# Kernel optimization log

Hardware: AMD Instinct MI355X
Metric: run time of the kernel (lower is better)

## Reference

```python
import jax, jax.numpy as jnp
import numpy as np

N = 300000   # total nodes
C = 32       # hidden states
M = 64       # discrete label alphabet
NGEN = 8     # number of generative models
G = 8192     # number of graphs


def setup_inputs() -> dict:
    key = jax.random.key(0)
    k1, k2, k3, k4 = jax.random.split(key, 4)
    B = jax.random.uniform(k1, (C, M, NGEN), minval=-5.0, maxval=5.0, dtype=jnp.float32)
    Pi = jax.random.uniform(k2, (C, NGEN), minval=-5.0, maxval=5.0, dtype=jnp.float32)
    x = jax.random.randint(k3, (N,), 0, M)
    batch = jnp.sort(jax.random.randint(k4, (N,), 0, G))
    return {"B": B, "Pi": Pi, "x": x, "batch": batch, "num_graphs": G}


def reference(B, Pi, x, batch, num_graphs):
    # softmax reparameterization: over M for B, over C for Pi (per generator)
    sm_B = jax.nn.softmax(B, axis=1)          # (C, M, n_gen)
    sm_Pi = jax.nn.softmax(Pi, axis=0)        # (C, n_gen)
    # gather per-node emission probs, then joint with prior -> (N, C, n_gen)
    numerator = sm_Pi[None, :, :] * jnp.transpose(sm_B[:, x, :], (1, 0, 2))
    posterior = numerator / numerator.sum(axis=1, keepdims=True)  # (N, C, n_gen)
    likelihood = (posterior * jnp.log(numerator)).sum(axis=1)     # (N, n_gen)
    # scatter-sum per graph
    likelihood = jax.ops.segment_sum(likelihood, batch, num_segments=num_graphs)  # (G, n_gen)
    h_vals = posterior.max(axis=1, keepdims=True)   # (N, 1, n_gen)
    h_idx = posterior.argmax(axis=1)                # (N, n_gen)
    return likelihood, h_vals, h_idx
```

## Files before the change

kernel.cpp:

```cpp
#include <hip/hip_runtime.h>

#define C_DIM 32
#define M_DIM 64
#define NG    8
#define TAB   (M_DIM * NG)
#define ST    9
#define BST   520
#define SPB   2048

__global__ void __launch_bounds__(512)
cgmm_prep(const float* __restrict__ B, const float* __restrict__ Pi,
          const int* __restrict__ batch,
          float* __restrict__ tab, int* __restrict__ starts,
          int N, int G, int nsb) {
    const int tid = threadIdx.x;

    if ((int)blockIdx.x < nsb) {
        const int base = blockIdx.x * SPB;
        for (int i = tid; i < SPB; i += 512) {
            const int n = base + i;
            if (n >= N) break;
            const int bn = batch[n];
            if (n == 0) {
                for (int j = 0; j <= bn; ++j) starts[j] = 0;
            } else {
                const int bp = batch[n - 1];
                for (int j = bp + 1; j <= bn; ++j) starts[j] = n;
            }
            if (n == N - 1) {
                for (int j = bn + 1; j <= G; ++j) starts[j] = N;
            }
        }
        return;
    }

    __shared__ float Bs[C_DIM * BST];
    __shared__ float Pis[C_DIM * NG];
    __shared__ float lsePi_s[NG];
    __shared__ float K_s[C_DIM * NG];

    {
        const float4* B4 = (const float4*)B;
        float4* Bs4 = (float4*)Bs;
        #pragma unroll
        for (int i = tid; i < (C_DIM * M_DIM * NG) / 4; i += 512) {
            Bs4[(i >> 7) * (BST / 4) + (i & 127)] = B4[i];
        }
        if (tid < C_DIM * NG / 4) ((float4*)Pis)[tid] = ((const float4*)Pi)[tid];
    }
    __syncthreads();

    if (tid < NG) {
        float mx = -1e30f;
        #pragma unroll
        for (int c = 0; c < C_DIM; ++c) mx = fmaxf(mx, Pis[c * NG + tid]);
        float s = 0.f;
        #pragma unroll
        for (int c = 0; c < C_DIM; ++c) s += expf(Pis[c * NG + tid] - mx);
        lsePi_s[tid] = logf(s) + mx;
    }
    __syncthreads();

    if (tid < C_DIM * NG) {
        const int c = tid >> 3, g = tid & 7;
        const float* bp = Bs + c * BST + g;
        float mx = -1e30f;
        #pragma unroll
        for (int m = 0; m < M_DIM; ++m) mx = fmaxf(mx, bp[m * NG]);
        float s = 0.f;
        #pragma unroll
        for (int m = 0; m < M_DIM; ++m) s += expf(bp[m * NG] - mx);
        K_s[tid] = Pis[tid] - (logf(s) + mx) - lsePi_s[g];
    }
    __syncthreads();

    {
        const int m = tid >> 3, g = tid & 7;
        float L[C_DIM];
        float best = -1e30f; int bidx = 0;
        #pragma unroll
        for (int c = 0; c < C_DIM; ++c) {
            float v = Bs[c * BST + m * NG + g] + K_s[c * NG + g];
            L[c] = v;
            if (v > best) { best = v; bidx = c; }
        }
        float se = 0.f, la = 0.f;
        #pragma unroll
        for (int c = 0; c < C_DIM; ++c) {
            float e = expf(L[c] - best);
            se += e; la += e * L[c];
        }
        tab[tid]           = la / se;
        tab[TAB + tid]     = 1.f / se;
        tab[2 * TAB + tid] = (float)bidx;
    }
}

__global__ void __launch_bounds__(256)
cgmm_write(const int* __restrict__ x, const int* __restrict__ starts,
           const float* __restrict__ tab,
           float* __restrict__ out_like, float* __restrict__ out_hv,
           float* __restrict__ out_hi, int G) {
    __shared__ float like_s[M_DIM * ST];
    __shared__ float hval_s[M_DIM * ST];
    __shared__ float hidx_s[M_DIM * ST];
    const int tid = threadIdx.x;
    for (int i = tid; i < TAB; i += 256) {
        const int p = (i >> 3) * ST + (i & 7);
        like_s[p] = tab[i];
        hval_s[p] = tab[TAB + i];
        hidx_s[p] = tab[2 * TAB + i];
    }
    __syncthreads();

    const int j = blockIdx.x * 4 + (tid >> 6);
    if (j >= G) return;
    const int start = starts[j];
    const int end   = starts[j + 1];

    const int slot = (tid >> 3) & 7;
    const int g    = tid & 7;

    float acc = 0.f;
    for (int n = start + slot; n < end; n += 8) {
        const int xm = x[n];
        const int p  = xm * ST + g;
        acc += like_s[p];
        out_hv[(size_t)n * NG + g] = hval_s[p];
        out_hi[(size_t)n * NG + g] = hidx_s[p];
    }
    acc += __shfl_xor(acc, 8);
    acc += __shfl_xor(acc, 16);
    acc += __shfl_xor(acc, 32);
    if ((tid & 63) < NG) out_like[(size_t)j * NG + g] = acc;
}

extern "C" void kernel_launch(void* const* d_in, const int* in_sizes, int n_in,
                              void* d_out, int out_size, void* d_ws, size_t ws_size,
                              hipStream_t stream) {
    const float* B     = (const float*)d_in[0];
    const float* Pi    = (const float*)d_in[1];
    const int*   x     = (const int*)d_in[2];
    const int*   batch = (const int*)d_in[3];
    const int N = in_sizes[2];
    const int G = (out_size - 2 * N * NG) / NG;

    float* tab    = (float*)d_ws;
    int*   starts = (int*)((char*)d_ws + 8192);

    float* out_like = (float*)d_out;
    float* out_hv   = out_like + (size_t)G * NG;
    float* out_hi   = out_hv + (size_t)N * NG;

    const int nsb = (N + SPB - 1) / SPB;

    cgmm_prep<<<nsb + 1, 512, 0, stream>>>(B, Pi, batch, tab, starts, N, G, nsb);
    cgmm_write<<<(G + 3) / 4, 256, 0, stream>>>(x, starts, tab, out_like,
                                                out_hv, out_hi, G);
}
```

Before: 19.98 us.

## Replace per-graph segment walk with per-node-block atomic segment reduction

Removes the segment-start computation pass and the per-graph write kernel. Instead, each block of 256 nodes reads x and batch, writes the per-node max and argmax outputs with coalesced stores, and does a run-length segment sum in LDS before adding into global likelihood with atomics. The prep kernel now zeroes the likelihood output in place of building starts. This balances work across nodes rather than graphs, at the cost of global float atomics and nondeterministic summation order.

```diff
diff --git a/kernel.cpp b/kernel.cpp
--- a/kernel.cpp
+++ b/kernel.cpp
@@ -6,31 +6,20 @@
 #define TAB   (M_DIM * NG)
 #define ST    9
 #define BST   520
-#define SPB   2048
+#define NPB   256
+#define KCH   8
 
 __global__ void __launch_bounds__(512)
 cgmm_prep(const float* __restrict__ B, const float* __restrict__ Pi,
-          const int* __restrict__ batch,
-          float* __restrict__ tab, int* __restrict__ starts,
-          int N, int G, int nsb) {
+          float* __restrict__ tab, float* __restrict__ out_like,
+          int G, int nzb) {
     const int tid = threadIdx.x;
 
-    if ((int)blockIdx.x < nsb) {
-        const int base = blockIdx.x * SPB;
-        for (int i = tid; i < SPB; i += 512) {
-            const int n = base + i;
-            if (n >= N) break;
-            const int bn = batch[n];
-            if (n == 0) {
-                for (int j = 0; j <= bn; ++j) starts[j] = 0;
-            } else {
-                const int bp = batch[n - 1];
-                for (int j = bp + 1; j <= bn; ++j) starts[j] = n;
-            }
-            if (n == N - 1) {
-                for (int j = bn + 1; j <= G; ++j) starts[j] = N;
-            }
-        }
+    if ((int)blockIdx.x < nzb) {
+        float4* z4 = (float4*)out_like;
+        const int nz4 = G * NG / 4;
+        for (int i = blockIdx.x * 512 + tid; i < nz4; i += nzb * 512)
+            z4[i] = make_float4(0.f, 0.f, 0.f, 0.f);
         return;
     }
 
@@ -43,9 +32,8 @@
         const float4* B4 = (const float4*)B;
         float4* Bs4 = (float4*)Bs;
         #pragma unroll
-        for (int i = tid; i < (C_DIM * M_DIM * NG) / 4; i += 512) {
+        for (int i = tid; i < (C_DIM * M_DIM * NG) / 4; i += 512)
             Bs4[(i >> 7) * (BST / 4) + (i & 127)] = B4[i];
-        }
         if (tid < C_DIM * NG / 4) ((float4*)Pis)[tid] = ((const float4*)Pi)[tid];
     }
     __syncthreads();
@@ -97,42 +85,70 @@
 }
 
 __global__ void __launch_bounds__(256)
-cgmm_write(const int* __restrict__ x, const int* __restrict__ starts,
+cgmm_nodes(const int* __restrict__ x, const int* __restrict__ batch,
            const float* __restrict__ tab,
            float* __restrict__ out_like, float* __restrict__ out_hv,
-           float* __restrict__ out_hi, int G) {
+           float* __restrict__ out_hi, int N) {
     __shared__ float like_s[M_DIM * ST];
     __shared__ float hval_s[M_DIM * ST];
     __shared__ float hidx_s[M_DIM * ST];
-    const int tid = threadIdx.x;
+    __shared__ int   xs_s[NPB];
+    __shared__ int   bs_s[NPB];
+    __shared__ float acc_ld[(NPB + 1) * NG];
+
+    const int tid  = threadIdx.x;
+    const int base = blockIdx.x * NPB;
+    const int nvalid = min(NPB, N - base);
+
     for (int i = tid; i < TAB; i += 256) {
         const int p = (i >> 3) * ST + (i & 7);
         like_s[p] = tab[i];
         hval_s[p] = tab[TAB + i];
         hidx_s[p] = tab[2 * TAB + i];
     }
+    if (tid < nvalid) {
+        xs_s[tid] = x[base + tid];
+        bs_s[tid] = batch[base + tid];
+    }
     __syncthreads();
 
-    const int j = blockIdx.x * 4 + (tid >> 6);
-    if (j >= G) return;
-    const int start = starts[j];
-    const int end   = starts[j + 1];
+    const int j0 = bs_s[0];
+    const int NJ = bs_s[nvalid - 1] - j0 + 1;
 
-    const int slot = (tid >> 3) & 7;
-    const int g    = tid & 7;
+    for (int i = tid; i < NJ * NG; i += 256) acc_ld[i] = 0.f;
 
-    float acc = 0.f;
-    for (int n = start + slot; n < end; n += 8) {
-        const int xm = x[n];
-        const int p  = xm * ST + g;
-        acc += like_s[p];
-        out_hv[(size_t)n * NG + g] = hval_s[p];
-        out_hi[(size_t)n * NG + g] = hidx_s[p];
+    const int s = tid >> 3, g = tid & 7;
+    #pragma unroll
+    for (int k = 0; k < NPB / 32; ++k) {
+        const int i = k * 32 + s;
+        if (i >= nvalid) break;
+        const int p = xs_s[i] * ST + g;
+        out_hv[(size_t)(base + i) * NG + g] = hval_s[p];
+        out_hi[(size_t)(base + i) * NG + g] = hidx_s[p];
     }
-    acc += __shfl_xor(acc, 8);
-    acc += __shfl_xor(acc, 16);
-    acc += __shfl_xor(acc, 32);
-    if ((tid & 63) < NG) out_like[(size_t)j * NG + g] = acc;
+    __syncthreads();
+
+    {
+        const int i0 = s * KCH;
+        float acc = 0.f;
+        int jprev = (i0 < nvalid) ? bs_s[i0] : -1;
+        #pragma unroll
+        for (int t = 0; t < KCH; ++t) {
+            const int i = i0 + t;
+            if (i >= nvalid) break;
+            const int j = bs_s[i];
+            if (j != jprev) {
+                atomicAdd(&acc_ld[(jprev - j0) * NG + g], acc);
+                acc = 0.f; jprev = j;
+            }
+            acc += like_s[xs_s[i] * ST + g];
+        }
+        if (jprev >= 0) atomicAdd(&acc_ld[(jprev - j0) * NG + g], acc);
+    }
+    __syncthreads();
+
+    for (int i = tid; i < NJ * NG; i += 256)
+        atomicAdd(&out_like[(size_t)j0 * NG + i], acc_ld[i]);
 }
 
 extern "C" void kernel_launch(void* const* d_in, const int* in_sizes, int n_in,
@@ -145,16 +161,15 @@
     const int N = in_sizes[2];
     const int G = (out_size - 2 * N * NG) / NG;
 
-    float* tab    = (float*)d_ws;
-    int*   starts = (int*)((char*)d_ws + 8192);
+    float* tab = (float*)d_ws;
 
     float* out_like = (float*)d_out;
     float* out_hv   = out_like + (size_t)G * NG;
     float* out_hi   = out_hv + (size_t)N * NG;
 
-    const int nsb = (N + SPB - 1) / SPB;
+    const int nzb = 8;
 
-    cgmm_prep<<<nsb + 1, 512, 0, stream>>>(B, Pi, batch, tab, starts, N, G, nsb);
-    cgmm_write<<<(G + 3) / 4, 256, 0, stream>>>(x, starts, tab, out_like,
-                                                out_hv, out_hi, G);
+    cgmm_prep<<<nzb + 1, 512, 0, stream>>>(B, Pi, tab, out_like, G, nzb);
+    cgmm_nodes<<<(N + NPB - 1) / NPB, 256, 0, stream>>>(x, batch, tab, out_like,
+                                                        out_hv, out_hi, N);
 }
```

Result: slower. 22.55 us (+12.9%).

## Split table prep across blocks and kernels with fast exp intrinsics

Applied to the files above, without the earlier changes.

Replaces the single-block softmax/table prep with a partials kernel that computes per-row exp sums across 32 blocks plus one Pi block, then a small tables kernel that builds the lookup table. The starts computation moves into the partials kernel with a smaller per-block span. It uses __expf/__logf and drops max subtraction, which shortens the serial critical path but removes overflow protection for large logits. It also adds an extra kernel launch.

```diff
diff --git a/kernel.cpp b/kernel.cpp
--- a/kernel.cpp
+++ b/kernel.cpp
@@ -5,95 +5,89 @@
 #define NG    8
 #define TAB   (M_DIM * NG)
 #define ST    9
-#define BST   520
-#define SPB   2048
+#define SPB   1024
 
-__global__ void __launch_bounds__(512)
-cgmm_prep(const float* __restrict__ B, const float* __restrict__ Pi,
-          const int* __restrict__ batch,
-          float* __restrict__ tab, int* __restrict__ starts,
-          int N, int G, int nsb) {
+
+__global__ void __launch_bounds__(256)
+cgmm_partials(const float* __restrict__ B, const float* __restrict__ Pi,
+              const int* __restrict__ batch,
+              float* __restrict__ Sexp, float* __restrict__ lsePi,
+              int* __restrict__ starts, int N, int G) {
     const int tid = threadIdx.x;
+    const int bid = blockIdx.x;
 
-    if ((int)blockIdx.x < nsb) {
-        const int base = blockIdx.x * SPB;
-        for (int i = tid; i < SPB; i += 512) {
-            const int n = base + i;
-            if (n >= N) break;
-            const int bn = batch[n];
-            if (n == 0) {
-                for (int j = 0; j <= bn; ++j) starts[j] = 0;
-            } else {
-                const int bp = batch[n - 1];
-                for (int j = bp + 1; j <= bn; ++j) starts[j] = n;
-            }
-            if (n == N - 1) {
-                for (int j = bn + 1; j <= G; ++j) starts[j] = N;
-            }
+    if (bid < C_DIM) {
+        __shared__ float row_s[M_DIM * NG];
+        const float* row = B + bid * (M_DIM * NG);
+        row_s[tid]       = row[tid];
+        row_s[tid + 256] = row[tid + 256];
+        __syncthreads();
+        if (tid < NG) {
+            float s = 0.f;
+            #pragma unroll
+            for (int m = 0; m < M_DIM; ++m) s += __expf(row_s[m * NG + tid]);
+            Sexp[bid * NG + tid] = s;
+        }
+        return;
+    }
+    if (bid == C_DIM) {
+        __shared__ float pi_s[C_DIM * NG];
+        pi_s[tid] = Pi[tid];
+        __syncthreads();
+        if (tid < NG) {
+            float s = 0.f;
+            #pragma unroll
+            for (int c = 0; c < C_DIM; ++c) s += __expf(pi_s[c * NG + tid]);
+            lsePi[tid] = __logf(s);
         }
         return;
     }
 
-    __shared__ float Bs[C_DIM * BST];
-    __shared__ float Pis[C_DIM * NG];
-    __shared__ float lsePi_s[NG];
+    const int base = (bid - C_DIM - 1) * SPB;
+    for (int i = tid; i < SPB; i += 256) {
+        const int n = base + i;
+        if (n >= N) break;
+        const int bn = batch[n];
+        if (n == 0) {
+            for (int j = 0; j <= bn; ++j) starts[j] = 0;
+        } else {
+            const int bp = batch[n - 1];
+            for (int j = bp + 1; j <= bn; ++j) starts[j] = n;
+        }
+        if (n == N - 1) {
+            for (int j = bn + 1; j <= G; ++j) starts[j] = N;
+        }
+    }
+}
+
+__global__ void __launch_bounds__(512)
+cgmm_tables(const float* __restrict__ B, const float* __restrict__ Pi,
+            const float* __restrict__ Sexp, const float* __restrict__ lsePi,
+            float* __restrict__ tab) {
     __shared__ float K_s[C_DIM * NG];
-
-    {
-        const float4* B4 = (const float4*)B;
-        float4* Bs4 = (float4*)Bs;
-        #pragma unroll
-        for (int i = tid; i < (C_DIM * M_DIM * NG) / 4; i += 512) {
-            Bs4[(i >> 7) * (BST / 4) + (i & 127)] = B4[i];
-        }
-        if (tid < C_DIM * NG / 4) ((float4*)Pis)[tid] = ((const float4*)Pi)[tid];
-    }
+    const int tid = threadIdx.x;
+    if (tid < C_DIM * NG)
+        K_s[tid] = Pi[tid] - __logf(Sexp[tid]) - lsePi[tid & 7];
     __syncthreads();
 
-    if (tid < NG) {
-        float mx = -1e30f;
-        #pragma unroll
-        for (int c = 0; c < C_DIM; ++c) mx = fmaxf(mx, Pis[c * NG + tid]);
-        float s = 0.f;
-        #pragma unroll
-        for (int c = 0; c < C_DIM; ++c) s += expf(Pis[c * NG + tid] - mx);
-        lsePi_s[tid] = logf(s) + mx;
+    const int g = tid & 7;
+    float L[C_DIM];
+    float best = -1e30f; int bidx = 0;
+    #pragma unroll
+    for (int c = 0; c < C_DIM; ++c) {
+        float v = B[c * (M_DIM * NG) + tid] + K_s[c * NG + g];
+        L[c] = v;
+        if (v > best) { best = v; bidx = c; }
     }
-    __syncthreads();
-
-    if (tid < C_DIM * NG) {
-        const int c = tid >> 3, g = tid & 7;
-        const float* bp = Bs + c * BST + g;
-        float mx = -1e30f;
-        #pragma unroll
-        for (int m = 0; m < M_DIM; ++m) mx = fmaxf(mx, bp[m * NG]);
-        float s = 0.f;
-        #pragma unroll
-        for (int m = 0; m < M_DIM; ++m) s += expf(bp[m * NG] - mx);
-        K_s[tid] = Pis[tid] - (logf(s) + mx) - lsePi_s[g];
+    float se = 0.f, la = 0.f;
+    #pragma unroll
+    for (int c = 0; c < C_DIM; ++c) {
+        float e = __expf(L[c] - best);
+        se += e; la += e * L[c];
     }
-    __syncthreads();
-
-    {
-        const int m = tid >> 3, g = tid & 7;
-        float L[C_DIM];
-        float best = -1e30f; int bidx = 0;
-        #pragma unroll
-        for (int c = 0; c < C_DIM; ++c) {
-            float v = Bs[c * BST + m * NG + g] + K_s[c * NG + g];
-            L[c] = v;
-            if (v > best) { best = v; bidx = c; }
-        }
-        float se = 0.f, la = 0.f;
-        #pragma unroll
-        for (int c = 0; c < C_DIM; ++c) {
-            float e = expf(L[c] - best);
-            se += e; la += e * L[c];
-        }
-        tab[tid]           = la / se;
-        tab[TAB + tid]     = 1.f / se;
-        tab[2 * TAB + tid] = (float)bidx;
-    }
+    tab[tid]           = la / se;
+    tab[TAB + tid]     = 1.f / se;
+    tab[2 * TAB + tid] = (float)bidx;
 }
 
 __global__ void __launch_bounds__(256)
@@ -146,7 +140,9 @@
     const int G = (out_size - 2 * N * NG) / NG;
 
     float* tab    = (float*)d_ws;
-    int*   starts = (int*)((char*)d_ws + 8192);
+    float* Sexp   = (float*)((char*)d_ws + 8192);
+    float* lsePi  = (float*)((char*)d_ws + 9216);
+    int*   starts = (int*)((char*)d_ws + 16384);
 
     float* out_like = (float*)d_out;
     float* out_hv   = out_like + (size_t)G * NG;
@@ -154,7 +150,9 @@
 
     const int nsb = (N + SPB - 1) / SPB;
 
-    cgmm_prep<<<nsb + 1, 512, 0, stream>>>(B, Pi, batch, tab, starts, N, G, nsb);
+    cgmm_partials<<<C_DIM + 1 + nsb, 256, 0, stream>>>(B, Pi, batch, Sexp,
+                                                       lsePi, starts, N, G);
+    cgmm_tables<<<1, 512, 0, stream>>>(B, Pi, Sexp, lsePi, tab);
     cgmm_write<<<(G + 3) / 4, 256, 0, stream>>>(x, starts, tab, out_like,
                                                 out_hv, out_hi, G);
 }
```

Result: no change. 20.03 us (+0.2%).
